# Performance work log

Hardware: AMD Instinct MI355X
Metric: run time of the kernel (lower is better)

The kernel has to match this reference:

```python
import jax, jax.numpy as jnp
import numpy as np

WINDOW = 512
STEP = WINDOW // 2


def hamming_window(n):
    # torch.hamming_window default is periodic=True: 0.54 - 0.46*cos(2*pi*k/n)
    return (0.54 - 0.46 * jnp.cos(2.0 * jnp.pi * jnp.arange(n) / n)).astype(jnp.float32)


def fft_convolve(a, b):
    # ortho-normalized rfft spectra, irfft, crop back to n samples.
    n = a.shape[-1]
    pa = jnp.pad(a, [(0, 0)] * (a.ndim - 1) + [(0, n)])
    pb = jnp.pad(b, [(0, 0)] * (b.ndim - 1) + [(0, n)])
    spec = jnp.fft.rfft(pa, axis=-1, norm='ortho') * jnp.fft.rfft(pb, axis=-1, norm='ortho')
    return jnp.fft.irfft(spec, n=2 * n, axis=-1, norm='ortho')[..., :n]


def fft_shift(a, shift):
    # repo's fft_shift: fractional shift via phase ramp in rfft domain of the
    n = a.shape[-1]
    shift_samples = shift * n * 0.5  # [..., 1]
    pa = jnp.pad(a, [(0, 0)] * (a.ndim - 1) + [(0, n)])
    spec = jnp.fft.rfft(pa, axis=-1, norm='ortho')  # [..., n+1]
    n_coeffs = spec.shape[-1]
    ramp = (jnp.arange(n_coeffs) * 2j * jnp.pi) / n_coeffs
    phase = jnp.exp(-ramp * shift_samples)  # broadcast over last dim
    return jnp.fft.irfft(spec * phase, n=2 * n, axis=-1, norm='ortho')


def setup_inputs() -> dict:
    key = jax.random.key(0)
    k1, k2 = jax.random.split(key)
    B, n = 4, 32768
    recon = jax.random.normal(k1, (B, 1, n), dtype=jnp.float32)
    target = jax.random.normal(k2, (B, 1, n), dtype=jnp.float32)
    return {"recon": recon, "target": target}


def reference(recon, target):
    batch = recon.shape[0]
    n_samples = recon.shape[-1]
    n_frames = (n_samples - WINDOW) // STEP + 1  # unfold(-1, 512, 256)

    # unfold: gather overlapping frames [B, n_frames, WINDOW]
    idx = jnp.arange(n_frames)[:, None] * STEP + jnp.arange(WINDOW)[None, :]
    frames = recon[:, 0, :][:, idx]  # [B, n_frames, WINDOW]
    windowed = (frames * hamming_window(WINDOW))[:, None, :, :]  # [B,1,F,W]

    # zero-pad each frame up to n_samples (the torch.cat with zeros)
    windowed = jnp.pad(windowed, ((0, 0), (0, 0), (0, 0), (0, n_samples - WINDOW)))

    # FFT cross-correlation surrogate against the full target
    fm = fft_convolve(windowed, target[:, :, None, :])[..., :n_samples]  # [B,1,F,n]

    positions = jnp.argmax(fm, axis=-1, keepdims=True).astype(jnp.float32) / n_samples

    positioned = fft_shift(windowed, positions)[..., :n_samples]  # [B,1,F,n]
    positioned = jnp.sum(positioned, axis=2).reshape(batch, 1, n_samples)

    return jnp.mean((positioned - target) ** 2)
```

## Files before the change

kernel.cpp:

```cpp
#include <hip/hip_runtime.h>
#include <math.h>

#define N_SAMP   32768
#define WINDOW   512
#define STEP     256
#define NFRAMES  127
#define NB       4
#define RTRUNC   1280
#define NSLAB    32
#define BPAD     776
#define HW       3104
#define VSTRIDE  193

#define WS_WF   0
#define WS_WFH  260096
#define WS_WFL  391168
#define WS_PV   522240
#define WS_M    587776
#define WS_CNT  588288
#define WS_LIST 588304
#define WS_H    592400
#define WS_PART 2169232

typedef _Float16 f16x8 __attribute__((ext_vector_type(8)));
typedef float f32x16 __attribute__((ext_vector_type(16)));

#define SW(L) ((L) ^ (((L) >> 3) & 7))

#define FMA4(A, LO, HI)                                           \
    A.x = fmaf(c.x, HI.x, A.x); A.x = fmaf(c.y, LO.w, A.x);       \
    A.x = fmaf(c.z, LO.z, A.x); A.x = fmaf(c.w, LO.y, A.x);       \
    A.y = fmaf(c.x, HI.y, A.y); A.y = fmaf(c.y, HI.x, A.y);       \
    A.y = fmaf(c.z, LO.w, A.y); A.y = fmaf(c.w, LO.z, A.y);       \
    A.z = fmaf(c.x, HI.z, A.z); A.z = fmaf(c.y, HI.y, A.z);       \
    A.z = fmaf(c.z, HI.x, A.z); A.z = fmaf(c.w, LO.w, A.z);       \
    A.w = fmaf(c.x, HI.w, A.w); A.w = fmaf(c.y, HI.z, A.w);       \
    A.w = fmaf(c.z, HI.y, A.w); A.w = fmaf(c.w, HI.x, A.w);

__global__ __launch_bounds__(256) void k_wf(const float* __restrict__ recon,
                                            float* __restrict__ wf,
                                            _Float16* __restrict__ wfh,
                                            float* __restrict__ part,
                                            int nslab) {
    int e = blockIdx.x * 256 + threadIdx.x;
    int w     = e & 511;
    int bf128 = e >> 9;
    int f = bf128 & 127;
    int b = bf128 >> 7;
    float val = 0.f;
    if (f < NFRAMES) {
        float ham = 0.54f - 0.46f * (float)cos((double)w * (M_PI / 256.0));
        val = ham * recon[b * N_SAMP + f * STEP + w];
        wf[(b * NFRAMES + f) * 512 + w] = val;
    }
    size_t tr = (((size_t)b * 64 + (w >> 3)) * 128 + f) * 8 + (w & 7);
    wfh[tr] = (_Float16)val;
    float4* p4 = (float4*)part;
    int nq = nslab * 32768;
    for (int q = e; q < nq; q += 262144)
        p4[q] = make_float4(0.f, 0.f, 0.f, 0.f);
}

__global__ __launch_bounds__(256, 4) void k_argmax_mfma(
        const float* __restrict__ tgt,
        const _Float16* __restrict__ wfh,
        float* __restrict__ pv) {
    __shared__ _Float16 sbh[8 * BPAD];
    __shared__ __align__(16) float stf[768];
    const int tid   = threadIdx.x;
    const int chunk = blockIdx.x & 127;
    const int half  = (blockIdx.x >> 7) & 1;
    const int b     = blockIdx.x >> 8;
    const int T0    = chunk * 256;
    const int TB    = T0 + 255;
    const float* tb = tgt + b * N_SAMP;

    if (tid < 192) {
        int A = TB - 767 + 4 * tid;
        float4 vq = (A >= 0) ? *(const float4*)(tb + A)
                             : make_float4(0.f, 0.f, 0.f, 0.f);
        *(float4*)(stf + 4 * tid) = vq;
    }
    __syncthreads();
    for (int oc = tid; oc < 768; oc += 256) {
        int r = oc / 96, s = oc - r * 96;
        int y0 = 767 - r - 8 * s;
        _Float16 h8[8];
#pragma unroll
        for (int j = 0; j < 8; ++j)
            h8[j] = (_Float16)stf[y0 - j];
        *(f16x8*)&sbh[r * BPAD + 8 * s] = *(f16x8*)h8;
    }
    __syncthreads();

    const int wv  = tid >> 6;
    const int q   = (tid >> 5) & 1;
    const int cl  = tid & 31;
    const int nt0 = 2 * wv;
    const int rp  = 7 - (cl & 7);
    const _Float16* Ah0 = wfh + ((size_t)b * 64) * 1024 + (half * 64 + cl) * 8;

    f32x16 acc00 = (f32x16)(0.f);
    f32x16 acc01 = (f32x16)(0.f);
    f32x16 acc10 = (f32x16)(0.f);
    f32x16 acc11 = (f32x16)(0.f);

    int off = q * 1024;
    int ea  = rp * BPAD + (255 - 32 * nt0 - cl + 8 * q - rp);
    f16x8 a0  = *(const f16x8*)(Ah0 + off);
    f16x8 a1  = *(const f16x8*)(Ah0 + off + 256);
    f16x8 bh0 = *(const f16x8*)&sbh[ea];
    f16x8 bh1 = *(const f16x8*)&sbh[ea - 32];
#pragma unroll
    for (int k0 = 0; k0 < 512; k0 += 16) {
        f16x8 a0n  = *(const f16x8*)(Ah0 + off + 2048);
        f16x8 a1n  = *(const f16x8*)(Ah0 + off + 2304);
        f16x8 bh0n = *(const f16x8*)&sbh[ea + 16];
        f16x8 bh1n = *(const f16x8*)&sbh[ea - 16];
        acc00 = __builtin_amdgcn_mfma_f32_32x32x16_f16(a0, bh0, acc00, 0, 0, 0);
        acc01 = __builtin_amdgcn_mfma_f32_32x32x16_f16(a0, bh1, acc01, 0, 0, 0);
        acc10 = __builtin_amdgcn_mfma_f32_32x32x16_f16(a1, bh0, acc10, 0, 0, 0);
        acc11 = __builtin_amdgcn_mfma_f32_32x32x16_f16(a1, bh1, acc11, 0, 0, 0);
        a0 = a0n; a1 = a1n; bh0 = bh0n; bh1 = bh1n;
        off += 2048; ea += 16;
    }

    __syncthreads();
    float* sval = (float*)sbh;
#pragma unroll
    for (int r = 0; r < 16; ++r) {
        float v0 = fmaxf(acc00[r], acc01[r]);
        float v1 = fmaxf(acc10[r], acc11[r]);
#pragma unroll
        for (int mm = 1; mm <= 16; mm <<= 1) {
            v0 = fmaxf(v0, __shfl_xor(v0, mm));
            v1 = fmaxf(v1, __shfl_xor(v1, mm));
        }
        if (cl == 0) {
            int row = (r & 3) + 8 * (r >> 2) + 4 * q;
            sval[row * 4 + wv]        = v0;
            sval[(32 + row) * 4 + wv] = v1;
        }
    }
    __syncthreads();
    if (tid < 64) {
        float v = fmaxf(fmaxf(sval[tid * 4], sval[tid * 4 + 1]),
                        fmaxf(sval[tid * 4 + 2], sval[tid * 4 + 3]));
        pv[((size_t)b * 128 + half * 64 + tid) * 128 + chunk] = v;
    }
}

__global__ __launch_bounds__(256) void k_vmax_coef(const float* __restrict__ tgt,
                                                   const float* __restrict__ wf,
                                                   const float* __restrict__ pv,
                                                   int* __restrict__ marr,
                                                   float* __restrict__ hbuf) {
    __shared__ __align__(16) float stg[4 * VSTRIDE * 4];
    __shared__ float rv[256];
    __shared__ int   ri[256];
    __shared__ int   clist[32];
    __shared__ int   ccnt;
    const int tid  = threadIdx.x;
    const int lane = tid & 63;
    const int wv   = tid >> 6;
    const int fr   = blockIdx.x;
    const int b    = fr / NFRAMES;
    const int f    = fr - b * NFRAMES;
    const float* prow = pv + ((size_t)b * 128 + f) * 128;
    const float* tb   = tgt + b * N_SAMP;
    const float4* wcg = (const float4*)(wf + (size_t)fr * 512);

    float mv = (tid < 128) ? prow[tid] : -3.4e38f;
    rv[tid] = mv;
    __syncthreads();
    for (int s = 128; s > 0; s >>= 1) {
        if (tid < s) rv[tid] = fmaxf(rv[tid], rv[tid + s]);
        __syncthreads();
    }
    float m0 = rv[0];
    if (tid == 0) ccnt = 0;
    __syncthreads();
    float eps = 0.012f * fabsf(m0) + 1e-3f;
    if (tid < 128 && mv >= m0 - eps) {
        int k = atomicAdd(&ccnt, 1);
        if (k < 32) clist[k] = tid;
    }
    __syncthreads();
    int nc = ccnt;
    int total = (nc <= 32) ? nc : 128;
    float bestv = -3.4e38f; int bestt = 0x7fffffff;
    float* myg = stg + wv * (VSTRIDE * 4);

    for (int ci = wv; ci < total; ci += 4) {
        int c2 = (nc <= 32) ? clist[ci] : ci;
        int T0 = c2 * 256;
        for (int e = lane; e < 192; e += 64) {
            int A = T0 - 512 + 4 * e;
            float4 vq = (A >= 0 && A < N_SAMP) ? *(const float4*)(tb + A)
                                               : make_float4(0.f, 0.f, 0.f, 0.f);
            *(float4*)(myg + 4 * e) = vq;
        }
        float4 acc = make_float4(0.f, 0.f, 0.f, 0.f);
        float4 lo = *(const float4*)(myg + 4 * (lane + 127));
        float4 hi = *(const float4*)(myg + 4 * (lane + 128));
        for (int g = 0; g < 127; ++g) {
            float4 nl = *(const float4*)(myg + 4 * (lane + 126 - g));
            const float4 c = wcg[g];
            FMA4(acc, lo, hi);
            hi = lo; lo = nl;
        }
        {
            const float4 c = wcg[127];
            FMA4(acc, lo, hi);
        }
        int tt = T0 + 4 * lane;
        if (acc.x > bestv || (acc.x == bestv && tt     < bestt)) { bestv = acc.x; bestt = tt;     }
        if (acc.y > bestv || (acc.y == bestv && tt + 1 < bestt)) { bestv = acc.y; bestt = tt + 1; }
        if (acc.z > bestv || (acc.z == bestv && tt + 2 < bestt)) { bestv = acc.z; bestt = tt + 2; }
        if (acc.w > bestv || (acc.w == bestv && tt + 3 < bestt)) { bestv = acc.w; bestt = tt + 3; }
    }
    rv[tid] = bestv; ri[tid] = bestt;
    __syncthreads();
    for (int s = 128; s > 0; s >>= 1) {
        if (tid < s) {
            float v2 = rv[tid + s]; int i2 = ri[tid + s];
            if (v2 > rv[tid] || (v2 == rv[tid] && i2 < ri[tid])) {
                rv[tid] = v2; ri[tid] = i2;
            }
        }
        __syncthreads();
    }
    int m = ri[0];
    if (tid == 0) marr[fr] = m;

    const double invD = 1.0 / 2147549184.0;
    const float  sd   = 4.7936899603827e-05f;
    const float  trf  = (float)(RTRUNC + 4) / 65536.0f;
    int p = (int)rint((double)m * (32768.0 / 32769.0));
    int jlo = p - (RTRUNC + 8); if (jlo < -512) jlo = -512; jlo &= ~3;
    float* hr = hbuf + (size_t)fr * HW;
    if (m == 0) {
        for (int k4 = tid; k4 < 776; k4 += 256) {
            int j0 = jlo + 4 * k4;
            float4 vq = make_float4((j0 == 0) ? 1.0f : 0.0f, 0.f, 0.f, 0.f);
            *(float4*)(hr + 4 * k4) = vq;
        }
        return;
    }
    double md32768 = (double)m * 32768.0;
    double sp = sin((double)m * (M_PI / 32769.0));
    float Cp = (float)(sp * (1.0 / 65536.0));
    if (m & 1) Cp = -Cp;
    float Cn = -Cp;
    for (int k4 = tid; k4 < 776; k4 += 256) {
        int j0 = jlo + 4 * k4;
        double A0 = (double)j0 * 32769.0 - md32768;
        double rA0 = A0 * invD;
        float f0v = (float)(rA0 - rint(rA0));
        float4 vq;
        if (fabsf(f0v) > trf) {
            vq = make_float4(0.f, 0.f, 0.f, 0.f);
        } else if (fabsf(f0v) < 6.2e-5f) {
#pragma unroll
            for (int k = 0; k < 4; ++k) {
                double rA = (A0 + (double)k * 32769.0) * invD;
                float ff = (float)(rA - rint(rA));
                float r2;
                if (ff == 0.0f) r2 = 65535.0f;
                else {
                    float s, c2;
                    __sincosf((float)M_PI * ff, &s, &c2);
                    r2 = c2 * __builtin_amdgcn_rcpf(s);
                }
                ((float*)&vq)[k] = ((k & 1) ? Cn : Cp) * r2;
            }
        } else {
            float s, c2;
            __sincosf((float)M_PI * f0v, &s, &c2);
            vq.x = Cp * (c2 * __builtin_amdgcn_rcpf(s));
            float s1 = fmaf(c2, sd, s);
            float c1 = fmaf(-s, sd, c2);
            vq.y = Cn * (c1 * __builtin_amdgcn_rcpf(s1));
            float s2 = fmaf(c1, sd, s1);
            float cc2 = fmaf(-s1, sd, c1);
            vq.z = Cp * (cc2 * __builtin_amdgcn_rcpf(s2));
            float s3 = fmaf(cc2, sd, s2);
            float c3 = fmaf(-s2, sd, cc2);
            vq.w = Cn * (c3 * __builtin_amdgcn_rcpf(s3));
        }
        *(float4*)(hr + 4 * k4) = vq;
    }
}

__global__ __launch_bounds__(256) void k_sched(const int* __restrict__ marr,
                                               int* __restrict__ list,
                                               int* __restrict__ cnt,
                                               int nslab,
                                               float* __restrict__ out) {
    __shared__ int scnt[64];
    __shared__ int total;
    const int tid = threadIdx.x;
    if (tid == 0) out[0] = 0.0f;
    if (tid < 64) scnt[tid] = 0;
    if (tid == 0) total = 0;
    __syncthreads();
    const int RT8 = RTRUNC + 8;
    for (int bf = tid; bf < NB * NFRAMES; bf += 256) {
        int b = bf / NFRAMES;
        int m = marr[bf];
        int p = (int)rint((double)m * (32768.0 / 32769.0));
        int lo = p - RT8;        if (lo < 0) lo = 0;
        int hi = p + RT8 + 511;  if (hi > N_SAMP - 1) hi = N_SAMP - 1;
        int r0 = lo >> 11, r1 = hi >> 11;
        for (int r = r0; r <= r1; ++r) {
            int bc = (b << 4) | r;
            int s = atomicAdd(&scnt[bc], 1);
            int k = atomicAdd(&total, 1);
            list[k] = (bf << 16) | (r << 8) | s;
        }
    }
    __syncthreads();
    int n = total;
    for (int k = tid; k < n; k += 256) {
        int v = list[k];
        int bf = (v >> 16) & 0x3fff;
        int r = (v >> 8) & 15;
        int b = bf / NFRAMES;
        if (scnt[(b << 4) | r] > nslab) list[k] = v | (1 << 30);
    }
    if (tid == 0) {
        int mx = 0;
        for (int i = 0; i < 64; ++i) mx = (scnt[i] > mx) ? scnt[i] : mx;
        cnt[0] = n;
        cnt[1] = (mx > nslab) ? nslab : mx;
    }
}

#define LDB(nn) (*(const float4*)(s_h + 4 * SW(nn)))

__global__ __launch_bounds__(256, 8) void k_shift_acc(const float* __restrict__ wf,
                                                      const int* __restrict__ marr,
                                                      const int* __restrict__ list,
                                                      const int* __restrict__ cnt,
                                                      const float* __restrict__ hbuf,
                                                      float* __restrict__ part,
                                                      int slabmask) {
    __shared__ __align__(16) float s_h[2560];
    const int tid = threadIdx.x;
    const int Lt  = 2 * tid;
    const int Ltw = (tid >> 6) * 128;
    const int n   = cnt[0];

    for (int se = blockIdx.x; se < n; se += gridDim.x) {
        int v     = list[se];
        int bf    = (v >> 16) & 0x3fff;
        int r     = (v >> 8) & 15;
        int slot  = v & 255;
        int isat  = (v >> 30) & 1;
        int b     = bf / NFRAMES;
        int t0s   = r << 11;
        const float4* __restrict__ wc = (const float4*)(wf + bf * 512);

        int m  = marr[bf];
        int pr = (int)rint((double)m * (32768.0 / 32769.0));
        int jlo = pr - (RTRUNC + 8); if (jlo < -512) jlo = -512; jlo &= ~3;
        int kb0 = ((t0s - 512) - jlo) >> 2;
        const float4* __restrict__ hb = (const float4*)(hbuf + (size_t)bf * HW);

        __syncthreads();
        for (int e4 = tid; e4 < 640; e4 += 256) {
            int kb = kb0 + e4;
            float4 vq = (kb >= 0 && kb < 776) ? hb[kb]
                                              : make_float4(0.f, 0.f, 0.f, 0.f);
            *(float4*)(s_h + 4 * SW(e4)) = vq;
        }
        __syncthreads();

        int blo = (pr - (RTRUNC + 8) - (t0s - 512)) >> 2;
        int bhi = (pr + (RTRUNC + 8) - (t0s - 512)) >> 2;
        if (blo < 0) blo = 0;
        if (bhi > 639) bhi = 639;

        float4 acc0 = make_float4(0.f, 0.f, 0.f, 0.f);
        float4 acc1 = acc0;

        int gmin = Ltw + 127 - bhi; if (gmin < 0) gmin = 0;
        int gmax = Ltw + 255 - blo; if (gmax > 127) gmax = 127;
        if (gmin <= gmax) {
            int gb0 = (gmin / 5) * 5;
            float4 s1v = LDB(Lt + 126 - gb0);
            float4 s2v = LDB(Lt + 127 - gb0);
            float4 s3v = LDB(Lt + 128 - gb0);
            float4 s4v = LDB(Lt + 129 - gb0);
            float4 s0v = s1v;
            int gend = (gmax < 120) ? gmax : 120;
            for (int gb = gb0; gb <= gend; gb += 5) {
                float4 t0 = LDB(Lt + 125 - gb);
                { const float4 c = wc[gb];     FMA4(acc0, s2v, s3v); FMA4(acc1, s3v, s4v); }
                s0v = t0;
                float4 t1 = LDB(Lt + 124 - gb);
                { const float4 c = wc[gb + 1]; FMA4(acc0, s1v, s2v); FMA4(acc1, s2v, s3v); }
                s4v = t1;
                float4 t2 = LDB(Lt + 123 - gb);
                { const float4 c = wc[gb + 2]; FMA4(acc0, s0v, s1v); FMA4(acc1, s1v, s2v); }
                s3v = t2;
                float4 t3 = LDB(Lt + 122 - gb);
                { const float4 c = wc[gb + 3]; FMA4(acc0, s4v, s0v); FMA4(acc1, s0v, s1v); }
                s2v = t3;
                float4 t4 = LDB(Lt + 121 - gb);
                { const float4 c = wc[gb + 4]; FMA4(acc0, s3v, s4v); FMA4(acc1, s4v, s0v); }
                s1v = t4;
            }
            if (gmax >= 125) {
                float4 t0 = LDB(Lt);
                { const float4 c = wc[125]; FMA4(acc0, s2v, s3v); FMA4(acc1, s3v, s4v); }
                s0v = t0;
                { const float4 c = wc[126]; FMA4(acc0, s1v, s2v); FMA4(acc1, s2v, s3v); }
                { const float4 c = wc[127]; FMA4(acc0, s0v, s1v); FMA4(acc1, s1v, s2v); }
            }
        }

        int slab = slot & slabmask;
        float* ob = part + (size_t)slab * (NB * N_SAMP) + b * N_SAMP + t0s;
        if (!isat) {
            *(float4*)(ob + 8 * tid)     = acc0;
            *(float4*)(ob + 8 * tid + 4) = acc1;
        } else {
            float* p0 = ob + 8 * tid;
            atomicAdd(p0 + 0, acc0.x); atomicAdd(p0 + 1, acc0.y);
            atomicAdd(p0 + 2, acc0.z); atomicAdd(p0 + 3, acc0.w);
            atomicAdd(p0 + 4, acc1.x); atomicAdd(p0 + 5, acc1.y);
            atomicAdd(p0 + 6, acc1.z); atomicAdd(p0 + 7, acc1.w);
        }
    }
}

__global__ __launch_bounds__(256) void k_mse(const float* __restrict__ part,
                                             const float* __restrict__ tgt,
                                             float* __restrict__ out,
                                             const int* __restrict__ cnt,
                                             int nslab) {
    __shared__ float sred[4];
    int e = blockIdx.x * 256 + threadIdx.x;
    int ng = cnt[1];
    if (ng > nslab) ng = nslab;
    float s0 = 0.f, s1 = 0.f, s2 = 0.f, s3 = 0.f;
    int g = 0;
    for (; g + 4 <= ng; g += 4) {
        s0 += part[(size_t)(g + 0) * (NB * N_SAMP) + e];
        s1 += part[(size_t)(g + 1) * (NB * N_SAMP) + e];
        s2 += part[(size_t)(g + 2) * (NB * N_SAMP) + e];
        s3 += part[(size_t)(g + 3) * (NB * N_SAMP) + e];
    }
    for (; g < ng; ++g)
        s0 += part[(size_t)g * (NB * N_SAMP) + e];
    float s = (s0 + s1) + (s2 + s3);
    float d = s - tgt[e];
    float v = d * d;
#pragma unroll
    for (int off = 32; off > 0; off >>= 1) v += __shfl_down(v, off, 64);
    int lane = threadIdx.x & 63, wid = threadIdx.x >> 6;
    if (lane == 0) sred[wid] = v;
    __syncthreads();
    if (threadIdx.x == 0) {
        float sm = sred[0] + sred[1] + sred[2] + sred[3];
        atomicAdd(out, sm * (1.0f / 131072.0f));
    }
}

extern "C" void kernel_launch(void* const* d_in, const int* in_sizes, int n_in,
                              void* d_out, int out_size, void* d_ws, size_t ws_size,
                              hipStream_t stream) {
    const float* recon = (const float*)d_in[0];
    const float* tgt   = (const float*)d_in[1];
    float* out = (float*)d_out;
    float* W   = (float*)d_ws;

    float*     wf   = W + WS_WF;
    _Float16*  wfh  = (_Float16*)(W + WS_WFH);
    float*     pv   = W + WS_PV;
    int*       marr = (int*)(W + WS_M);
    int*       cnt  = (int*)(W + WS_CNT);
    int*       list = (int*)(W + WS_LIST);
    float*     hbuf = W + WS_H;
    float*     part = W + WS_PART;

    int nslab = NSLAB;
    while (nslab > 1 &&
           ((size_t)WS_PART + (size_t)nslab * NB * N_SAMP) * sizeof(float) > ws_size)
        nslab >>= 1;

    k_wf<<<1024, 256, 0, stream>>>(recon, wf, wfh, part, nslab);
    k_argmax_mfma<<<1024, 256, 0, stream>>>(tgt, wfh, pv);
    k_vmax_coef<<<NB * NFRAMES, 256, 0, stream>>>(tgt, wf, pv, marr, hbuf);
    k_sched<<<1, 256, 0, stream>>>(marr, list, cnt, nslab, out);
    k_shift_acc<<<2048, 256, 0, stream>>>(wf, marr, list, cnt, hbuf, part, nslab - 1);
    k_mse<<<512, 256, 0, stream>>>(part, tgt, out, cnt, nslab);
}
```

Measured before the change: 154.5 us.

## Replace slab partial buffers with direct atomic accumulation into one output buffer

Drops the per-slot slab buffers (up to 32 copies of the signal), their zeroing in k_wf, and the multi-slab reduction in k_mse. Every shift-accumulate tile now atomically adds straight into a single B×N buffer, which also simplifies k_sched. This cuts memory traffic for zeroing and reducing, at the cost of more atomic contention on overlapping tiles. The argmax refinement loop also gains a deeper register prefetch of shared-memory operands.

```diff
diff --git a/kernel.cpp b/kernel.cpp
--- a/kernel.cpp
+++ b/kernel.cpp
@@ -7,10 +7,10 @@
 #define NFRAMES  127
 #define NB       4
 #define RTRUNC   1280
-#define NSLAB    32
 #define BPAD     776
 #define HW       3104
 #define VSTRIDE  193
+#define LISTCAP  4096
 
 #define WS_WF   0
 #define WS_WFH  260096
@@ -20,7 +20,7 @@
 #define WS_CNT  588288
 #define WS_LIST 588304
 #define WS_H    592400
-#define WS_PART 2169232
+#define WS_OUT  2169232
 
 typedef _Float16 f16x8 __attribute__((ext_vector_type(8)));
 typedef float f32x16 __attribute__((ext_vector_type(16)));
@@ -40,8 +40,7 @@
 __global__ __launch_bounds__(256) void k_wf(const float* __restrict__ recon,
                                             float* __restrict__ wf,
                                             _Float16* __restrict__ wfh,
-                                            float* __restrict__ part,
-                                            int nslab) {
+                                            float* __restrict__ outbuf) {
     int e = blockIdx.x * 256 + threadIdx.x;
     int w     = e & 511;
     int bf128 = e >> 9;
@@ -55,10 +54,8 @@
     }
     size_t tr = (((size_t)b * 64 + (w >> 3)) * 128 + f) * 8 + (w & 7);
     wfh[tr] = (_Float16)val;
-    float4* p4 = (float4*)part;
-    int nq = nslab * 32768;
-    for (int q = e; q < nq; q += 262144)
-        p4[q] = make_float4(0.f, 0.f, 0.f, 0.f);
+    if (e < 32768)
+        ((float4*)outbuf)[e] = make_float4(0.f, 0.f, 0.f, 0.f);
 }
 
 __global__ __launch_bounds__(256, 4) void k_argmax_mfma(
@@ -191,6 +188,7 @@
     float bestv = -3.4e38f; int bestt = 0x7fffffff;
     float* myg = stg + wv * (VSTRIDE * 4);
 
+#define MYG(x) (*(const float4*)(myg + 4 * (lane + (x))))
     for (int ci = wv; ci < total; ci += 4) {
         int c2 = (nc <= 32) ? clist[ci] : ci;
         int T0 = c2 * 256;
@@ -201,24 +199,23 @@
             *(float4*)(myg + 4 * e) = vq;
         }
         float4 acc = make_float4(0.f, 0.f, 0.f, 0.f);
-        float4 lo = *(const float4*)(myg + 4 * (lane + 127));
-        float4 hi = *(const float4*)(myg + 4 * (lane + 128));
-        for (int g = 0; g < 127; ++g) {
-            float4 nl = *(const float4*)(myg + 4 * (lane + 126 - g));
+        float4 lo = MYG(127), hi = MYG(128), n1 = MYG(126), n2 = MYG(125);
+        for (int g = 0; g < 125; ++g) {
+            float4 nf = MYG(124 - g);
             const float4 c = wcg[g];
             FMA4(acc, lo, hi);
-            hi = lo; lo = nl;
-        }
-        {
-            const float4 c = wcg[127];
-            FMA4(acc, lo, hi);
-        }
+            hi = lo; lo = n1; n1 = n2; n2 = nf;
+        }
+        { const float4 c = wcg[125]; FMA4(acc, lo, hi); hi = lo; lo = n1; n1 = n2; }
+        { const float4 c = wcg[126]; FMA4(acc, lo, hi); hi = lo; lo = n1; }
+        { const float4 c = wcg[127]; FMA4(acc, lo, hi); }
         int tt = T0 + 4 * lane;
         if (acc.x > bestv || (acc.x == bestv && tt     < bestt)) { bestv = acc.x; bestt = tt;     }
         if (acc.y > bestv || (acc.y == bestv && tt + 1 < bestt)) { bestv = acc.y; bestt = tt + 1; }
         if (acc.z > bestv || (acc.z == bestv && tt + 2 < bestt)) { bestv = acc.z; bestt = tt + 2; }
         if (acc.w > bestv || (acc.w == bestv && tt + 3 < bestt)) { bestv = acc.w; bestt = tt + 3; }
     }
+#undef MYG
     rv[tid] = bestv; ri[tid] = bestt;
     __syncthreads();
     for (int s = 128; s > 0; s >>= 1) {
@@ -295,45 +292,25 @@
 __global__ __launch_bounds__(256) void k_sched(const int* __restrict__ marr,
                                                int* __restrict__ list,
                                                int* __restrict__ cnt,
-                                               int nslab,
                                                float* __restrict__ out) {
-    __shared__ int scnt[64];
     __shared__ int total;
     const int tid = threadIdx.x;
-    if (tid == 0) out[0] = 0.0f;
-    if (tid < 64) scnt[tid] = 0;
-    if (tid == 0) total = 0;
+    if (tid == 0) { out[0] = 0.0f; total = 0; }
     __syncthreads();
     const int RT8 = RTRUNC + 8;
     for (int bf = tid; bf < NB * NFRAMES; bf += 256) {
-        int b = bf / NFRAMES;
         int m = marr[bf];
         int p = (int)rint((double)m * (32768.0 / 32769.0));
         int lo = p - RT8;        if (lo < 0) lo = 0;
         int hi = p + RT8 + 511;  if (hi > N_SAMP - 1) hi = N_SAMP - 1;
         int r0 = lo >> 11, r1 = hi >> 11;
         for (int r = r0; r <= r1; ++r) {
-            int bc = (b << 4) | r;
-            int s = atomicAdd(&scnt[bc], 1);
             int k = atomicAdd(&total, 1);
-            list[k] = (bf << 16) | (r << 8) | s;
-        }
-    }
-    __syncthreads();
-    int n = total;
-    for (int k = tid; k < n; k += 256) {
-        int v = list[k];
-        int bf = (v >> 16) & 0x3fff;
-        int r = (v >> 8) & 15;
-        int b = bf / NFRAMES;
-        if (scnt[(b << 4) | r] > nslab) list[k] = v | (1 << 30);
-    }
-    if (tid == 0) {
-        int mx = 0;
-        for (int i = 0; i < 64; ++i) mx = (scnt[i] > mx) ? scnt[i] : mx;
-        cnt[0] = n;
-        cnt[1] = (mx > nslab) ? nslab : mx;
-    }
+            list[k] = (bf << 16) | (r << 8);
+        }
+    }
+    __syncthreads();
+    if (tid == 0) cnt[0] = total;
 }
 
 #define LDB(nn) (*(const float4*)(s_h + 4 * SW(nn)))
@@ -343,8 +320,7 @@
                                                       const int* __restrict__ list,
                                                       const int* __restrict__ cnt,
                                                       const float* __restrict__ hbuf,
-                                                      float* __restrict__ part,
-                                                      int slabmask) {
+                                                      float* __restrict__ outbuf) {
     __shared__ __align__(16) float s_h[2560];
     const int tid = threadIdx.x;
     const int Lt  = 2 * tid;
@@ -355,8 +331,6 @@
         int v     = list[se];
         int bf    = (v >> 16) & 0x3fff;
         int r     = (v >> 8) & 15;
-        int slot  = v & 255;
-        int isat  = (v >> 30) & 1;
         int b     = bf / NFRAMES;
         int t0s   = r << 11;
         const float4* __restrict__ wc = (const float4*)(wf + bf * 512);
@@ -420,42 +394,20 @@
             }
         }
 
-        int slab = slot & slabmask;
-        float* ob = part + (size_t)slab * (NB * N_SAMP) + b * N_SAMP + t0s;
-        if (!isat) {
-            *(float4*)(ob + 8 * tid)     = acc0;
-            *(float4*)(ob + 8 * tid + 4) = acc1;
-        } else {
-            float* p0 = ob + 8 * tid;
-            atomicAdd(p0 + 0, acc0.x); atomicAdd(p0 + 1, acc0.y);
-            atomicAdd(p0 + 2, acc0.z); atomicAdd(p0 + 3, acc0.w);
-            atomicAdd(p0 + 4, acc1.x); atomicAdd(p0 + 5, acc1.y);
-            atomicAdd(p0 + 6, acc1.z); atomicAdd(p0 + 7, acc1.w);
-        }
-    }
-}
-
-__global__ __launch_bounds__(256) void k_mse(const float* __restrict__ part,
+        float* p0 = outbuf + b * N_SAMP + t0s + 8 * tid;
+        atomicAdd(p0 + 0, acc0.x); atomicAdd(p0 + 1, acc0.y);
+        atomicAdd(p0 + 2, acc0.z); atomicAdd(p0 + 3, acc0.w);
+        atomicAdd(p0 + 4, acc1.x); atomicAdd(p0 + 5, acc1.y);
+        atomicAdd(p0 + 6, acc1.z); atomicAdd(p0 + 7, acc1.w);
+    }
+}
+
+__global__ __launch_bounds__(256) void k_mse(const float* __restrict__ outbuf,
                                              const float* __restrict__ tgt,
-                                             float* __restrict__ out,
-                                             const int* __restrict__ cnt,
-                                             int nslab) {
+                                             float* __restrict__ out) {
     __shared__ float sred[4];
     int e = blockIdx.x * 256 + threadIdx.x;
-    int ng = cnt[1];
-    if (ng > nslab) ng = nslab;
-    float s0 = 0.f, s1 = 0.f, s2 = 0.f, s3 = 0.f;
-    int g = 0;
-    for (; g + 4 <= ng; g += 4) {
-        s0 += part[(size_t)(g + 0) * (NB * N_SAMP) + e];
-        s1 += part[(size_t)(g + 1) * (NB * N_SAMP) + e];
-        s2 += part[(size_t)(g + 2) * (NB * N_SAMP) + e];
-        s3 += part[(size_t)(g + 3) * (NB * N_SAMP) + e];
-    }
-    for (; g < ng; ++g)
-        s0 += part[(size_t)g * (NB * N_SAMP) + e];
-    float s = (s0 + s1) + (s2 + s3);
-    float d = s - tgt[e];
+    float d = outbuf[e] - tgt[e];
     float v = d * d;
 #pragma unroll
     for (int off = 32; off > 0; off >>= 1) v += __shfl_down(v, off, 64);
@@ -483,17 +435,12 @@
     int*       cnt  = (int*)(W + WS_CNT);
     int*       list = (int*)(W + WS_LIST);
     float*     hbuf = W + WS_H;
-    float*     part = W + WS_PART;
-
-    int nslab = NSLAB;
-    while (nslab > 1 &&
-           ((size_t)WS_PART + (size_t)nslab * NB * N_SAMP) * sizeof(float) > ws_size)
-        nslab >>= 1;
-
-    k_wf<<<1024, 256, 0, stream>>>(recon, wf, wfh, part, nslab);
+    float*     outbuf = W + WS_OUT;
+
+    k_wf<<<1024, 256, 0, stream>>>(recon, wf, wfh, outbuf);
     k_argmax_mfma<<<1024, 256, 0, stream>>>(tgt, wfh, pv);
     k_vmax_coef<<<NB * NFRAMES, 256, 0, stream>>>(tgt, wf, pv, marr, hbuf);
-    k_sched<<<1, 256, 0, stream>>>(marr, list, cnt, nslab, out);
-    k_shift_acc<<<2048, 256, 0, stream>>>(wf, marr, list, cnt, hbuf, part, nslab - 1);
-    k_mse<<<512, 256, 0, stream>>>(part, tgt, out, cnt, nslab);
-}
+    k_sched<<<1, 256, 0, stream>>>(marr, list, cnt, out);
+    k_shift_acc<<<2048, 256, 0, stream>>>(wf, marr, list, cnt, hbuf, outbuf);
+    k_mse<<<512, 256, 0, stream>>>(outbuf, tgt, out);
+}
```

Result: slower. 197.4 us (+27.7%).
